# Kernel optimization log

Measured on AMD Instinct MI355X. Metric: run time of the kernel, lower is better.

The kernel has to match this reference:

```python
import math
import jax, jax.numpy as jnp
import numpy as np

UNITS = 256
D_IN = 256
BATCH = 65536
STRENGTH = 0.5
PERIOD = 25.0
LAMBDA_SLOW = 0.1
JITTER = 0.05
H_INERTIA = 0.9
REST_BASELINE = 1.0


def setup_inputs() -> dict:
    key = jax.random.key(0)
    k1, k2, k3, k4, k5, k6 = jax.random.split(key, 6)
    glorot = math.sqrt(2.0 / (D_IN + UNITS))
    return {
        "inputs": jax.random.normal(k1, (BATCH, D_IN), dtype=jnp.float32),
        "prev_h": jax.random.normal(k2, (BATCH, UNITS), dtype=jnp.float32),
        "prev_G": jax.random.normal(k3, (BATCH, UNITS), dtype=jnp.float32),
        "prev_phase": jax.random.normal(k4, (BATCH, 1), dtype=jnp.float32),
        "w_in": jax.random.normal(k5, (D_IN, UNITS), dtype=jnp.float32) * glorot,
        "w_rec": jax.random.normal(k6, (UNITS, UNITS), dtype=jnp.float32) * (1.0 / math.sqrt(UNITS)),
        "bias": jnp.zeros((UNITS,), dtype=jnp.float32),
    }


def reference(inputs, prev_h, prev_G, prev_phase, w_in, w_rec, bias):
    half = UNITS // 2
    # roll-like swap of the two halves of the hidden state
    raw_signal = jnp.concatenate([prev_h[:, half:], prev_h[:, :half]], axis=1)
    # slow exponential-moving-average field
    new_G = (1.0 - LAMBDA_SLOW) * prev_G + LAMBDA_SLOW * raw_signal
    mean = jnp.mean(new_G, axis=-1, keepdims=True)
    std = jnp.std(new_G, axis=-1, keepdims=True)  # population std, matches tf.math.reduce_std
    G_norm = (new_G - mean) / (std + 1e-6)
    new_phase = prev_phase + 2.0 * math.pi / PERIOD
    oscillator = jnp.sin(new_phase)
    bias_signal = jnp.mean(raw_signal, axis=-1, keepdims=True) - 0.1
    combined_signal = oscillator + JITTER * bias_signal
    field_effect = REST_BASELINE + STRENGTH * combined_signal * jnp.tanh(G_norm)
    z = (inputs @ w_in + prev_h @ w_rec + bias) * field_effect
    h = H_INERTIA * prev_h + (1.0 - H_INERTIA) * jax.nn.elu(z)
    h = jnp.clip(h, -20.0, 20.0)
    return (h, new_G, new_phase)
```

## Files before the change

### kernel.cpp

```cpp
#include <hip/hip_runtime.h>

typedef unsigned short ushort_t;
typedef short v8s __attribute__((ext_vector_type(8)));
typedef float v4f __attribute__((ext_vector_type(4)));

#define BATCH    65536
#define UNITS    256
#define M_TILE   64
#define KSTEPS   16
#define BCHUNK   10240
#define T_STRIDE 264
#define LDS_HB   0
#define LDS_GT   33792
#define LDS_SC   67584
#define LDS_TOT  69376

__device__ __forceinline__ float b2f(ushort_t u) {
    union { unsigned int i; float f; } v; v.i = ((unsigned int)u) << 16; return v.f;
}
__device__ __forceinline__ ushort_t f2b(float f) {
    union { float f; unsigned int i; } v; v.f = f;
    unsigned int r = (v.i + 0x7fffu + ((v.i >> 16) & 1u)) >> 16;
    return (ushort_t)r;
}

__global__ void pack_w(const float* __restrict__ w_in,
                       const float* __restrict__ w_rec,
                       ushort_t* __restrict__ Wp) {
    int gid = blockIdx.x * 256 + threadIdx.x;
    int k = gid >> 8, n = gid & 255;
    float v = (k < 256) ? w_in[k * 256 + n] : w_rec[(k - 256) * 256 + n];
    Wp[(size_t)(k >> 5) * BCHUNK + n * 40 + (k & 31)] = f2b(v);
}

__global__ __launch_bounds__(256, 2)
void fused_cell(const float* __restrict__ inputs,
                const float* __restrict__ prev_h,
                const float* __restrict__ prev_G,
                const float* __restrict__ prev_phase,
                const ushort_t* __restrict__ Wp,
                const float* __restrict__ bias,
                float* __restrict__ out) {
    __shared__ __align__(16) char smem[LDS_TOT];
    short* Hb     = (short*)(smem + LDS_HB);
    short* Gt     = (short*)(smem + LDS_GT);
    float* r_mean = (float*)(smem + LDS_SC);
    float* r_rstd = r_mean + 64;
    float* r_comb = r_rstd + 64;
    float* bias_f = r_comb + 64;

    const int tid  = threadIdx.x;
    const int l    = tid & 63;
    const int w    = tid >> 6;
    const int row0 = blockIdx.x * M_TILE;

    float* outH = out;
    float* outG = out + (size_t)BATCH * UNITS;
    float* outP = out + (size_t)2 * BATCH * UNITS;

    bias_f[tid] = bias[tid];

    for (int rr = 0; rr < 16; ++rr) {
        int lr = w * 16 + rr;
        int gr = row0 + lr;
        int c0 = l * 4;
        int pc = (c0 + 128) & 255;
        float4 hp = *(const float4*)(prev_h + (size_t)gr * UNITS + pc);
        float4 gp = *(const float4*)(prev_G + (size_t)gr * UNITS + c0);
        float4 ng;
        ng.x = 0.9f * gp.x + 0.1f * hp.x;
        ng.y = 0.9f * gp.y + 0.1f * hp.y;
        ng.z = 0.9f * gp.z + 0.1f * hp.z;
        ng.w = 0.9f * gp.w + 0.1f * hp.w;
        float s1 = ng.x + ng.y + ng.z + ng.w;
        float s2 = ng.x*ng.x + ng.y*ng.y + ng.z*ng.z + ng.w*ng.w;
        float sh = hp.x + hp.y + hp.z + hp.w;
        *(float4*)(outG + (size_t)gr * UNITS + c0) = ng;
        ushort4 gq; gq.x = f2b(ng.x); gq.y = f2b(ng.y); gq.z = f2b(ng.z); gq.w = f2b(ng.w);
        *(ushort4*)(Gt + lr * T_STRIDE + c0) = gq;
        ushort4 hq; hq.x = f2b(hp.x); hq.y = f2b(hp.y); hq.z = f2b(hp.z); hq.w = f2b(hp.w);
        *(ushort4*)(Hb + lr * T_STRIDE + pc) = hq;
        #pragma unroll
        for (int off = 32; off > 0; off >>= 1) {
            s1 += __shfl_xor(s1, off, 64);
            s2 += __shfl_xor(s2, off, 64);
            sh += __shfl_xor(sh, off, 64);
        }
        if (l == 0) {
            float mean = s1 * (1.f / 256.f);
            float var  = s2 * (1.f / 256.f) - mean * mean;
            float rstd = 1.f / (sqrtf(fmaxf(var, 0.f)) + 1e-6f);
            float np   = prev_phase[gr] + 0.2513274122871834591f;
            outP[gr] = np;
            float comb = sinf(np) + 0.05f * (sh * (1.f / 256.f) - 0.1f);
            r_mean[lr] = mean; r_rstd[lr] = rstd; r_comb[lr] = comb;
        }
    }

    __syncthreads();

    const int n16 = l & 15;
    const int q   = l >> 4;
    v4f acc[16];
    const v4f z4 = {0.f, 0.f, 0.f, 0.f};
    #pragma unroll
    for (int t = 0; t < 16; ++t) acc[t] = z4;

    const int arow = w * 16 + n16;
    const float* ainp = inputs + (size_t)(row0 + arow) * UNITS + q * 8;
    const short* hbp  = Hb + arow * T_STRIDE + q * 8;
    const short* bp   = (const short*)Wp + n16 * 40 + q * 8;

    #pragma unroll 2
    for (int s = 0; s < KSTEPS; ++s) {
        v8s a;
        if (s < 8) {
            float4 f0 = *(const float4*)(ainp + s * 32);
            float4 f1 = *(const float4*)(ainp + s * 32 + 4);
            a[0] = (short)f2b(f0.x); a[1] = (short)f2b(f0.y);
            a[2] = (short)f2b(f0.z); a[3] = (short)f2b(f0.w);
            a[4] = (short)f2b(f1.x); a[5] = (short)f2b(f1.y);
            a[6] = (short)f2b(f1.z); a[7] = (short)f2b(f1.w);
        } else {
            a = *(const v8s*)(hbp + (s - 8) * 32);
        }
        const short* bs = bp + s * BCHUNK;
        #pragma unroll
        for (int t = 0; t < 16; ++t) {
            v8s b = *(const v8s*)(bs + t * 640);
            acc[t] = __builtin_amdgcn_mfma_f32_16x16x32_bf16(a, b, acc[t], 0, 0, 0);
        }
    }

    #pragma unroll
    for (int t = 0; t < 16; ++t) {
        int c = t * 16 + n16;
        float bz = bias_f[c];
        #pragma unroll
        for (int r = 0; r < 4; ++r) {
            int lr = w * 16 + q * 4 + r;
            int gr = row0 + lr;
            float gval = b2f((ushort_t)Gt[lr * T_STRIDE + c]);
            float gn = (gval - r_mean[lr]) * r_rstd[lr];
            float e2 = __expf(2.f * gn);
            float th = 1.f - 2.f / (e2 + 1.f);
            float field = 1.f + 0.5f * r_comb[lr] * th;
            float z = (acc[t][r] + bz) * field;
            float el = (z > 0.f) ? z : (__expf(z) - 1.f);
            float h = 0.9f * b2f((ushort_t)Hb[lr * T_STRIDE + c]) + 0.1f * el;
            h = fminf(fmaxf(h, -20.f), 20.f);
            outH[(size_t)gr * UNITS + c] = h;
        }
    }
}

extern "C" void kernel_launch(void* const* d_in, const int* in_sizes, int n_in,
                              void* d_out, int out_size, void* d_ws, size_t ws_size,
                              hipStream_t stream) {
    const float* inputs     = (const float*)d_in[0];
    const float* prev_h     = (const float*)d_in[1];
    const float* prev_G     = (const float*)d_in[2];
    const float* prev_phase = (const float*)d_in[3];
    const float* w_in       = (const float*)d_in[4];
    const float* w_rec      = (const float*)d_in[5];
    const float* bias       = (const float*)d_in[6];
    float* out    = (float*)d_out;
    ushort_t* Wp  = (ushort_t*)d_ws;

    pack_w<<<512, 256, 0, stream>>>(w_in, w_rec, Wp);
    fused_cell<<<BATCH / M_TILE, 256, 0, stream>>>(inputs, prev_h, prev_G,
                                                   prev_phase, Wp, bias, out);
}
```

Baseline: 344.2 us.

## Halve row tile to 32 and split columns across wave pairs for occupancy

Shrinks the per-block row tile from 64 to 32. The four waves are now arranged as two row groups times two column halves, so each wave holds 8 accumulator tiles instead of 16. The prologue is reworked so that 8 threads cooperate on each row with a short shuffle reduction, and launch bounds are raised to 4 blocks per SM, using smaller LDS and fewer registers to increase occupancy and latency hiding. In exchange, each A fragment (the fp32 input converted to bf16) is loaded and converted by two waves, and weight reads per output row double.

```diff
diff --git a/kernel.cpp b/kernel.cpp
--- a/kernel.cpp
+++ b/kernel.cpp
@@ -6,14 +6,14 @@
 
 #define BATCH    65536
 #define UNITS    256
-#define M_TILE   64
+#define M_TILE   32
 #define KSTEPS   16
 #define BCHUNK   10240
 #define T_STRIDE 264
 #define LDS_HB   0
-#define LDS_GT   33792
-#define LDS_SC   67584
-#define LDS_TOT  69376
+#define LDS_GT   16896
+#define LDS_SC   33792
+#define LDS_TOT  35200
 
 __device__ __forceinline__ float b2f(ushort_t u) {
     union { unsigned int i; float f; } v; v.i = ((unsigned int)u) << 16; return v.f;
@@ -33,7 +33,7 @@
     Wp[(size_t)(k >> 5) * BCHUNK + n * 40 + (k & 31)] = f2b(v);
 }
 
-__global__ __launch_bounds__(256, 2)
+__global__ __launch_bounds__(256, 4)
 void fused_cell(const float* __restrict__ inputs,
                 const float* __restrict__ prev_h,
                 const float* __restrict__ prev_G,
@@ -45,13 +45,11 @@
     short* Hb     = (short*)(smem + LDS_HB);
     short* Gt     = (short*)(smem + LDS_GT);
     float* r_mean = (float*)(smem + LDS_SC);
-    float* r_rstd = r_mean + 64;
-    float* r_comb = r_rstd + 64;
-    float* bias_f = r_comb + 64;
+    float* r_rstd = r_mean + 32;
+    float* r_comb = r_rstd + 32;
+    float* bias_f = r_comb + 32;
 
     const int tid  = threadIdx.x;
-    const int l    = tid & 63;
-    const int w    = tid >> 6;
     const int row0 = blockIdx.x * M_TILE;
 
     float* outH = out;
@@ -60,33 +58,38 @@
 
     bias_f[tid] = bias[tid];
 
-    for (int rr = 0; rr < 16; ++rr) {
-        int lr = w * 16 + rr;
-        int gr = row0 + lr;
-        int c0 = l * 4;
-        int pc = (c0 + 128) & 255;
-        float4 hp = *(const float4*)(prev_h + (size_t)gr * UNITS + pc);
-        float4 gp = *(const float4*)(prev_G + (size_t)gr * UNITS + c0);
-        float4 ng;
-        ng.x = 0.9f * gp.x + 0.1f * hp.x;
-        ng.y = 0.9f * gp.y + 0.1f * hp.y;
-        ng.z = 0.9f * gp.z + 0.1f * hp.z;
-        ng.w = 0.9f * gp.w + 0.1f * hp.w;
-        float s1 = ng.x + ng.y + ng.z + ng.w;
-        float s2 = ng.x*ng.x + ng.y*ng.y + ng.z*ng.z + ng.w*ng.w;
-        float sh = hp.x + hp.y + hp.z + hp.w;
-        *(float4*)(outG + (size_t)gr * UNITS + c0) = ng;
-        ushort4 gq; gq.x = f2b(ng.x); gq.y = f2b(ng.y); gq.z = f2b(ng.z); gq.w = f2b(ng.w);
-        *(ushort4*)(Gt + lr * T_STRIDE + c0) = gq;
-        ushort4 hq; hq.x = f2b(hp.x); hq.y = f2b(hp.y); hq.z = f2b(hp.z); hq.w = f2b(hp.w);
-        *(ushort4*)(Hb + lr * T_STRIDE + pc) = hq;
+    {
+        const int lr = tid >> 3;
+        const int p  = tid & 7;
+        const int gr = row0 + lr;
+        float s1 = 0.f, s2 = 0.f, sh = 0.f;
         #pragma unroll
-        for (int off = 32; off > 0; off >>= 1) {
+        for (int i = 0; i < 8; ++i) {
+            int c0 = i * 32 + p * 4;
+            int pc = (c0 + 128) & 255;
+            float4 hp = *(const float4*)(prev_h + (size_t)gr * UNITS + pc);
+            float4 gp = *(const float4*)(prev_G + (size_t)gr * UNITS + c0);
+            float4 ng;
+            ng.x = 0.9f * gp.x + 0.1f * hp.x;
+            ng.y = 0.9f * gp.y + 0.1f * hp.y;
+            ng.z = 0.9f * gp.z + 0.1f * hp.z;
+            ng.w = 0.9f * gp.w + 0.1f * hp.w;
+            s1 += ng.x + ng.y + ng.z + ng.w;
+            s2 += ng.x*ng.x + ng.y*ng.y + ng.z*ng.z + ng.w*ng.w;
+            sh += hp.x + hp.y + hp.z + hp.w;
+            *(float4*)(outG + (size_t)gr * UNITS + c0) = ng;
+            ushort4 gq; gq.x = f2b(ng.x); gq.y = f2b(ng.y); gq.z = f2b(ng.z); gq.w = f2b(ng.w);
+            *(ushort4*)(Gt + lr * T_STRIDE + c0) = gq;
+            ushort4 hq; hq.x = f2b(hp.x); hq.y = f2b(hp.y); hq.z = f2b(hp.z); hq.w = f2b(hp.w);
+            *(ushort4*)(Hb + lr * T_STRIDE + pc) = hq;
+        }
+        #pragma unroll
+        for (int off = 4; off > 0; off >>= 1) {
             s1 += __shfl_xor(s1, off, 64);
             s2 += __shfl_xor(s2, off, 64);
             sh += __shfl_xor(sh, off, 64);
         }
-        if (l == 0) {
+        if (p == 0) {
             float mean = s1 * (1.f / 256.f);
             float var  = s2 * (1.f / 256.f) - mean * mean;
             float rstd = 1.f / (sqrtf(fmaxf(var, 0.f)) + 1e-6f);
@@ -99,17 +102,22 @@
 
     __syncthreads();
 
+    const int l   = tid & 63;
+    const int w   = tid >> 6;
     const int n16 = l & 15;
     const int q   = l >> 4;
-    v4f acc[16];
+    const int rg  = w & 1;
+    const int ch  = w >> 1;
+
+    v4f acc[8];
     const v4f z4 = {0.f, 0.f, 0.f, 0.f};
     #pragma unroll
-    for (int t = 0; t < 16; ++t) acc[t] = z4;
+    for (int t = 0; t < 8; ++t) acc[t] = z4;
 
-    const int arow = w * 16 + n16;
+    const int arow = rg * 16 + n16;
     const float* ainp = inputs + (size_t)(row0 + arow) * UNITS + q * 8;
     const short* hbp  = Hb + arow * T_STRIDE + q * 8;
-    const short* bp   = (const short*)Wp + n16 * 40 + q * 8;
+    const short* bp   = (const short*)Wp + (ch * 128 + n16) * 40 + q * 8;
 
     #pragma unroll 2
     for (int s = 0; s < KSTEPS; ++s) {
@@ -126,19 +134,19 @@
         }
         const short* bs = bp + s * BCHUNK;
         #pragma unroll
-        for (int t = 0; t < 16; ++t) {
+        for (int t = 0; t < 8; ++t) {
             v8s b = *(const v8s*)(bs + t * 640);
             acc[t] = __builtin_amdgcn_mfma_f32_16x16x32_bf16(a, b, acc[t], 0, 0, 0);
         }
     }
 
     #pragma unroll
-    for (int t = 0; t < 16; ++t) {
-        int c = t * 16 + n16;
+    for (int t = 0; t < 8; ++t) {
+        int c = ch * 128 + t * 16 + n16;
         float bz = bias_f[c];
         #pragma unroll
         for (int r = 0; r < 4; ++r) {
-            int lr = w * 16 + q * 4 + r;
+            int lr = rg * 16 + q * 4 + r;
             int gr = row0 + lr;
             float gval = b2f((ushort_t)Gt[lr * T_STRIDE + c]);
             float gn = (gval - r_mean[lr]) * r_rstd[lr];
```

Result: faster. 329.3 us (-4.3%).
